# Kernel optimization log

Measured on AMD Instinct MI355X. Metric: run time of the kernel, lower is better.

Reference implementation:

```python
import jax, jax.numpy as jnp
import numpy as np

B, T, C, D, P = 8, 512, 32, 128, 1024
EPS = 1e-5

def setup_inputs() -> dict:
    key = jax.random.key(0)
    ks = jax.random.split(key, 11)
    s = 1.0 / np.sqrt(D)
    inp = {
        'x': jax.random.normal(ks[0], (B, T, C, D), jnp.float32),
        'x_mask': jax.random.randint(ks[1], (B, T, C), 0, 2) == 1,
        'p_mask': jax.random.randint(ks[2], (B, T, C), 0, 2) == 1,
        'pos': jax.random.randint(ks[3], (B, T, C), 0, P),
        'pe': jax.random.normal(ks[4], (P, D // 2, 2), jnp.float32),  # complex rpe as [re, im]
        'imp': jax.random.randint(ks[5], (B, T), 0, C),
        'idx_c': jax.random.randint(ks[6], (B, T, C), 0, C),
        'wq_w': jax.random.normal(ks[7], (D, D), jnp.float32) * s,
        'wq_b': jnp.zeros((D,), jnp.float32),
        'wk_w': jax.random.normal(ks[8], (D, D), jnp.float32) * s,
        'wk_b': jnp.zeros((D,), jnp.float32),
        'wv_w': jax.random.normal(ks[9], (D, D), jnp.float32) * s,
        'wv_b': jnp.zeros((D,), jnp.float32),
        'ls_gamma': 1e-5 * jnp.ones((D,), jnp.float32),
        'ln_gamma': jnp.ones((D,), jnp.float32),
        'ln_beta': jnp.zeros((D,), jnp.float32),
    }
    return inp


def _rotate(z, r):
    # z: (b,t,c,d) real; r: (b,t,c,d/2,2) complex multiplier [re,im]
    b, t, c, d = z.shape
    zr = z.reshape(b, t, c, d // 2, 2)
    re = zr[..., 0] * r[..., 0] - zr[..., 1] * r[..., 1]
    im = zr[..., 0] * r[..., 1] + zr[..., 1] * r[..., 0]
    return jnp.stack([re, im], axis=-1).reshape(b, t, c, d)


def reference(x, x_mask, p_mask, pos, pe, imp, idx_c,
              wq_w, wq_b, wk_w, wk_b, wv_w, wv_b,
              ls_gamma, ln_gamma, ln_beta):
    b, t, c, d = x.shape
    # channel selection gather: where x_mask, use per-token important channel
    imp_rep = jnp.broadcast_to(imp[:, :, None], (b, t, c))
    idx = jnp.where(x_mask, imp_rep, idx_c)            # (b,t,c)
    xg = jnp.take_along_axis(x, idx[..., None], axis=2)  # (b,t,c,d)
    # QKV projections (torch Linear: x @ W.T + b)
    q = xg @ wq_w.T + wq_b
    k = xg @ wk_w.T + wk_b
    v = xg @ wv_w.T + wv_b
    # relative PE complex rotation on q,k
    r = pe[pos]                                        # (b,t,c,d/2,2)
    q = _rotate(q, r)
    k = _rotate(k, r)
    # (b,c,t,d) layout; channel acts as head
    qt = q.transpose(0, 2, 1, 3)
    kt = k.transpose(0, 2, 1, 3)
    vt = v.transpose(0, 2, 1, 3)
    scores = jnp.einsum('bcqd,bckd->bcqk', qt, kt) / jnp.sqrt(jnp.float32(d))
    pm = p_mask.transpose(0, 2, 1)                     # (b,c,t)
    mask = pm[:, :, :, None] | pm[:, :, None, :]       # (b,c,t,t)
    attn = jax.nn.softmax(jnp.where(mask, -jnp.inf, scores), axis=-1)
    attn = jnp.nan_to_num(attn)
    xm = x_mask.transpose(0, 2, 1)                     # (b,c,t)
    weight = jnp.where(xm, 1.0 / t, 1.0)
    out = jnp.einsum('bcmn,bcnd->bmcd', attn * weight[:, :, None, :], vt)  # (b,t,c,d)
    # norm_first=False: LN(x + layer_scale(out))
    y = x + ls_gamma * out
    mu = jnp.mean(y, axis=-1, keepdims=True)
    var = jnp.mean(jnp.square(y - mu), axis=-1, keepdims=True)
    return (y - mu) / jnp.sqrt(var + EPS) * ln_gamma + ln_beta
```

## Files before the change

kernel.cpp:

```cpp
#include <hip/hip_runtime.h>
#include <hip/hip_bf16.h>

#define Bb 8
#define Tt 512
#define Cc 32
#define Dd 128
#define SCALE 0.08838834764831845f
#define SROW 520

typedef unsigned int u32;
typedef __hip_bfloat16 bf16;
typedef __attribute__((ext_vector_type(8))) short short8;
typedef __attribute__((ext_vector_type(4))) short short4v;
typedef __attribute__((ext_vector_type(4))) float floatx4;

__device__ __forceinline__ short f2bf(float f) {
    __hip_bfloat16 h = __float2bfloat16(f);
    return *(short*)&h;
}
__device__ __forceinline__ float bf2f(short s) {
    return __uint_as_float(((u32)(unsigned short)s) << 16);
}

__global__ __launch_bounds__(256)
void k_wconv(const float* __restrict__ wq, const float* __restrict__ wk,
             const float* __restrict__ wv, short* __restrict__ Wb)
{
    int g = blockIdx.x * 256 + threadIdx.x;
    int mat = g >> 14, rem = g & 16383;
    const float* src = (mat == 0) ? wq : (mat == 1) ? wk : wv;
    Wb[g] = f2bf(src[rem]);
}

__global__ __launch_bounds__(256)
void k_qkvm(const float* __restrict__ x, const int* __restrict__ xm,
            const int* __restrict__ pos, const float* __restrict__ pe,
            const int* __restrict__ imp, const int* __restrict__ idxc,
            const short* __restrict__ Wb,
            const float* __restrict__ bq, const float* __restrict__ bk,
            const float* __restrict__ bv,
            short* __restrict__ qb, short* __restrict__ kb, short* __restrict__ vb)
{
    const int R0  = blockIdx.x * 64;
    const int b   = R0 >> 14;
    const int t0  = (R0 >> 5) & 511;
    const int tid = threadIdx.x;
    const int w    = tid >> 6;
    const int lane = tid & 63;
    const int quad = lane >> 4;
    const int m    = lane & 15;

    __shared__ short xg[64 * 136];
    __shared__ short ot[64 * 392];

#pragma unroll
    for (int i = 0; i < 8; ++i) {
        int u   = tid + i * 256;
        int row = u >> 5, seg = u & 31;
        int R   = R0 + row;
        int idx = xm[R] ? imp[R >> 5] : idxc[R];
        float4 v = *(const float4*)(x + ((long)(R >> 5) * Cc + idx) * Dd + seg * 4);
        short4v s = {f2bf(v.x), f2bf(v.y), f2bf(v.z), f2bf(v.w)};
        *(short4v*)&xg[row * 136 + seg * 4] = s;
    }

    short8 wf[6][4];
    float  bias_v[6];
#pragma unroll
    for (int mat = 0; mat < 3; ++mat) {
        const float* bp = (mat == 0) ? bq : (mat == 1) ? bk : bv;
#pragma unroll
        for (int h = 0; h < 2; ++h) {
            int sl = mat * 2 + h;
            int ct = h * 4 + w;
            bias_v[sl] = bp[ct * 16 + m];
#pragma unroll
            for (int kk = 0; kk < 4; ++kk)
                wf[sl][kk] = *(const short8*)(Wb + ((long)mat * 128 + ct * 16 + m) * 128
                                              + kk * 32 + quad * 8);
        }
    }
    __syncthreads();

    for (int rt = 0; rt < 4; ++rt) {
        short8 af[4];
#pragma unroll
        for (int kk = 0; kk < 4; ++kk)
            af[kk] = *(const short8*)&xg[(rt * 16 + m) * 136 + kk * 32 + quad * 8];

        floatx4 acc[6];
#pragma unroll
        for (int sl = 0; sl < 6; ++sl) acc[sl] = (floatx4){0.f, 0.f, 0.f, 0.f};
#pragma unroll
        for (int kk = 0; kk < 4; ++kk)
#pragma unroll
            for (int sl = 0; sl < 6; ++sl)
                acc[sl] = __builtin_amdgcn_mfma_f32_16x16x32_bf16(af[kk], wf[sl][kk], acc[sl], 0, 0, 0);

        int po[4];
#pragma unroll
        for (int r = 0; r < 4; ++r) po[r] = pos[R0 + rt * 16 + quad * 4 + r];

#pragma unroll
        for (int sl = 0; sl < 6; ++sl) {
            int mat = sl >> 1;
            int ct  = (sl & 1) * 4 + w;
            int d   = ct * 16 + m;
#pragma unroll
            for (int r = 0; r < 4; ++r) {
                float v = acc[sl][r] + bias_v[sl];
                float p = __shfl_xor(v, 1, 64);
                if (mat < 2) {
                    const float* rp = pe + ((long)po[r] * (Dd / 2) + (d >> 1)) * 2;
                    float r0 = rp[0], r1 = rp[1];
                    v = (d & 1) ? fmaf(p, r1, v * r0) : fmaf(v, r0, -(p * r1));
                    if (mat == 0) v *= SCALE;
                }
                ot[(rt * 16 + quad * 4 + r) * 392 + mat * 128 + d] = f2bf(v);
            }
        }
    }
    __syncthreads();

    short* const mats[3] = {qb, kb, vb};
#pragma unroll
    for (int mat = 0; mat < 3; ++mat) {
        short* dst = mats[mat];
#pragma unroll
        for (int i = 0; i < 4; ++i) {
            int g = tid + i * 256;
            int n = g >> 4, off = (g & 15) * 8;
            int c = n & 31, tl = n >> 5;
            *(short8*)(dst + (((long)(b * Cc + c) * Tt) + t0 + tl) * Dd + off) =
                *(const short8*)&ot[n * 392 + mat * 128 + off];
        }
    }
}

__global__ __launch_bounds__(256)
void k_vt(const short* __restrict__ vb, const int* __restrict__ xm,
          short* __restrict__ vt)
{
    const int head = blockIdx.y;
    const int b    = head >> 5;
    const int c    = head & 31;
    const int t0   = blockIdx.x * 64;
    const int tid  = threadIdx.x;

    __shared__ short tile[64 * 136];
    __shared__ float wks[64];

    if (tid < 64)
        wks[tid] = xm[((long)b * Tt + t0 + tid) * Cc + c] ? (1.0f / Tt) : 1.0f;

    const short* src = vb + ((long)head * Tt + t0) * Dd;
#pragma unroll
    for (int i = 0; i < 4; ++i) {
        int u = tid + i * 256;
        int row = u >> 4, col8 = u & 15;
        int c8 = col8 ^ ((row >> 3) & 7);
        *(short8*)&tile[row * 136 + c8 * 8] = *(const short8*)(src + row * Dd + col8 * 8);
    }
    __syncthreads();

    short* dst = vt + (long)head * Dd * Tt + t0;
#pragma unroll
    for (int i = 0; i < 4; ++i) {
        int u = tid + i * 256;
        int d = u >> 3, t8 = (u & 7) * 8;
        int key = u & 7;
        int cs = ((d >> 3) ^ key) * 8 + (d & 7);
        short8 v;
#pragma unroll
        for (int j = 0; j < 8; ++j)
            v[j] = f2bf(bf2f(tile[(t8 + j) * 136 + cs]) * wks[t8 + j]);
        *(short8*)(dst + (long)d * Tt + t8) = v;
    }
}

__global__ __launch_bounds__(512, 4)
void k_attn(const short* __restrict__ qb, const short* __restrict__ kbp,
            const short* __restrict__ vtp, const float* __restrict__ x,
            const int* __restrict__ pm,
            const float* __restrict__ lsg, const float* __restrict__ lng,
            const float* __restrict__ lnb, float* __restrict__ out)
{
    const int l    = blockIdx.y * 256 + blockIdx.x;
    const int xcd  = l & 7;
    const int sws  = l >> 3;
    const int hh   = sws & 7;
    const int tl   = (sws >> 3) & 7;
    const int gg   = sws >> 6;
    const int head = xcd + ((gg * 8 + hh) << 3);
    const int b    = head >> 5;
    const int c    = head & 31;
    const int qt0  = tl * 64;
    const int tid  = threadIdx.x;
    const int w    = tid >> 6;
    const int lane = tid & 63;
    const int quad = lane >> 4;
    const int m    = lane & 15;

    __shared__ short S[64 * SROW];
    __shared__ u32   pkbits[16];
    __shared__ float rlS[64];
    __shared__ float ps1[8][64];
    __shared__ float ps2[8][64];
    __shared__ float mrs[64][2];

    {
        bool v = pm[((long)b * Tt + tid) * Cc + c] != 0;
        unsigned long long bal = __ballot(v);
        if (lane == 0) {
            pkbits[w * 2]     = (u32)bal;
            pkbits[w * 2 + 1] = (u32)(bal >> 32);
        }
    }

    short8 qf[4][4];
#pragma unroll
    for (int qt = 0; qt < 4; ++qt)
#pragma unroll
        for (int kk = 0; kk < 4; ++kk)
            qf[qt][kk] = *(const short8*)(qb + ((long)head * Tt + qt0 + qt * 16 + m) * Dd
                                          + kk * 32 + quad * 8);
    __syncthreads();

    for (int ch = 0; ch < 4; ++ch) {
        int kt = ch * 128 + w * 16 + m;
        const short* kp = kbp + ((long)head * Tt + kt) * Dd + quad * 8;
        floatx4 sc[4];
#pragma unroll
        for (int qt = 0; qt < 4; ++qt) sc[qt] = (floatx4){0.f, 0.f, 0.f, 0.f};
#pragma unroll
        for (int kk = 0; kk < 4; ++kk) {
            short8 bk = *(const short8*)(kp + kk * 32);
#pragma unroll
            for (int qt = 0; qt < 4; ++qt)
                sc[qt] = __builtin_amdgcn_mfma_f32_16x16x32_bf16(qf[qt][kk], bk, sc[qt], 0, 0, 0);
        }
        bool masked = (pkbits[kt >> 5] >> (kt & 31)) & 1;
#pragma unroll
        for (int qt = 0; qt < 4; ++qt)
#pragma unroll
            for (int r = 0; r < 4; ++r)
                S[(qt * 16 + quad * 4 + r) * SROW + kt] = f2bf(masked ? -1e30f : sc[qt][r]);
    }
    __syncthreads();

    {
        int qi = tid >> 3, part = tid & 7;
        short* rowp = &S[qi * SROW + part * 8];
        short8 sv[8];
#pragma unroll
        for (int j = 0; j < 8; ++j) sv[j] = *(short8*)&rowp[j * 64];
        float mx = -1e30f;
#pragma unroll
        for (int j = 0; j < 8; ++j)
#pragma unroll
            for (int e = 0; e < 8; ++e) mx = fmaxf(mx, bf2f(sv[j][e]));
        mx = fmaxf(mx, __shfl_xor(mx, 1, 64));
        mx = fmaxf(mx, __shfl_xor(mx, 2, 64));
        mx = fmaxf(mx, __shfl_xor(mx, 4, 64));
        float lsum = 0.f;
#pragma unroll
        for (int j = 0; j < 8; ++j)
#pragma unroll
            for (int e = 0; e < 8; ++e) {
                float s = bf2f(sv[j][e]);
                float ex = (s <= -1e29f) ? 0.f : __expf(s - mx);
                sv[j][e] = f2bf(ex);
                lsum += ex;
            }
#pragma unroll
        for (int j = 0; j < 8; ++j) *(short8*)&rowp[j * 64] = sv[j];
        lsum += __shfl_xor(lsum, 1, 64);
        lsum += __shfl_xor(lsum, 2, 64);
        lsum += __shfl_xor(lsum, 4, 64);
        if (part == 0) {
            int t = qt0 + qi;
            bool qmask = (pkbits[t >> 5] >> (t & 31)) & 1;
            rlS[qi] = (lsum > 0.f && !qmask) ? 1.0f / lsum : 0.f;
        }
    }
    __syncthreads();

    floatx4 oa[4];
#pragma unroll
    for (int qt = 0; qt < 4; ++qt) oa[qt] = (floatx4){0.f, 0.f, 0.f, 0.f};

    const short* vbase = vtp + (long)head * Dd * Tt + ((long)(w * 16 + m)) * Tt + quad * 8;
    for (int kv = 0; kv < 16; ++kv) {
        short8 bv = *(const short8*)(vbase + kv * 32);
#pragma unroll
        for (int qt = 0; qt < 4; ++qt) {
            short8 ap = *(const short8*)&S[(qt * 16 + m) * SROW + kv * 32 + quad * 8];
            oa[qt] = __builtin_amdgcn_mfma_f32_16x16x32_bf16(ap, bv, oa[qt], 0, 0, 0);
        }
    }

    const int d = w * 16 + m;
    const float lg = lsg[d];
    float yv[4][4];
    float s1[4][4], s2[4][4];
#pragma unroll
    for (int qt = 0; qt < 4; ++qt)
#pragma unroll
        for (int r = 0; r < 4; ++r) {
            int row = qt * 16 + quad * 4 + r;
            int t = qt0 + row;
            float val = oa[qt][r] * rlS[row];
            float y = x[(((long)b * Tt + t) * Cc + c) * Dd + d] + lg * val;
            yv[qt][r] = y;
            s1[qt][r] = y;
            s2[qt][r] = y * y;
        }
#pragma unroll
    for (int qt = 0; qt < 4; ++qt)
#pragma unroll
        for (int r = 0; r < 4; ++r) {
            float a = s1[qt][r], bb = s2[qt][r];
            a += __shfl_xor(a, 1, 64); bb += __shfl_xor(bb, 1, 64);
            a += __shfl_xor(a, 2, 64); bb += __shfl_xor(bb, 2, 64);
            a += __shfl_xor(a, 4, 64); bb += __shfl_xor(bb, 4, 64);
            a += __shfl_xor(a, 8, 64); bb += __shfl_xor(bb, 8, 64);
            if (m == 0) {
                ps1[w][qt * 16 + quad * 4 + r] = a;
                ps2[w][qt * 16 + quad * 4 + r] = bb;
            }
        }
    __syncthreads();
    if (tid < 64) {
        float a = 0.f, bb = 0.f;
#pragma unroll
        for (int wv = 0; wv < 8; ++wv) { a += ps1[wv][tid]; bb += ps2[wv][tid]; }
        float mean = a * (1.0f / Dd);
        float var  = bb * (1.0f / Dd) - mean * mean;
        mrs[tid][0] = mean;
        mrs[tid][1] = rsqrtf(var + 1e-5f);
    }
    __syncthreads();

    const float g = lng[d], be = lnb[d];
#pragma unroll
    for (int qt = 0; qt < 4; ++qt)
#pragma unroll
        for (int r = 0; r < 4; ++r) {
            int row = qt * 16 + quad * 4 + r;
            int t = qt0 + row;
            out[(((long)b * Tt + t) * Cc + c) * Dd + d] =
                (yv[qt][r] - mrs[row][0]) * mrs[row][1] * g + be;
        }
}

extern "C" void kernel_launch(void* const* d_in, const int* in_sizes, int n_in,
                              void* d_out, int out_size, void* d_ws, size_t ws_size,
                              hipStream_t stream) {
    const float* x    = (const float*)d_in[0];
    const int* xmask  = (const int*)d_in[1];
    const int* pmask  = (const int*)d_in[2];
    const int* pos    = (const int*)d_in[3];
    const float* pe   = (const float*)d_in[4];
    const int* imp    = (const int*)d_in[5];
    const int* idxc   = (const int*)d_in[6];
    const float* wq_w = (const float*)d_in[7];
    const float* wq_b = (const float*)d_in[8];
    const float* wk_w = (const float*)d_in[9];
    const float* wk_b = (const float*)d_in[10];
    const float* wv_w = (const float*)d_in[11];
    const float* wv_b = (const float*)d_in[12];
    const float* lsg  = (const float*)d_in[13];
    const float* lng  = (const float*)d_in[14];
    const float* lnb  = (const float*)d_in[15];
    float* out = (float*)d_out;

    size_t n = (size_t)Bb * Cc * Tt * Dd;
    short* qb = (short*)d_ws;
    short* kb = qb + n;
    short* vb = kb + n;
    short* vt = vb + n;
    short* Wb = vt + n;

    k_wconv<<<dim3(3 * Dd * Dd / 256), dim3(256), 0, stream>>>(wq_w, wk_w, wv_w, Wb);
    k_qkvm<<<dim3(Bb * Tt * Cc / 64), dim3(256), 0, stream>>>(
        x, xmask, pos, pe, imp, idxc, Wb, wq_b, wk_b, wv_b, qb, kb, vb);
    k_vt<<<dim3(Tt / 64, Bb * Cc), dim3(256), 0, stream>>>(vb, xmask, vt);
    k_attn<<<dim3(256, 8), dim3(512), 0, stream>>>(
        qb, kb, vt, x, pmask, lsg, lng, lnb, out);
}
```

Before: 313.5 us.

## Split attention over two key halves with online softmax to halve LDS score buffer

Processes keys in two halves of 256, keeping a running max and sum per query row and rescaling the output accumulator between halves, so the shared score tile shrinks by half. The aim is to let more blocks reside per CU by reducing LDS usage, and the launch bounds are raised accordingly. It adds extra barriers and rescale work, and the tighter launch bounds may pressure registers.

After: 588.9 us. +87.8%, slower.

```diff
diff --git a/kernel.cpp b/kernel.cpp
--- a/kernel.cpp
+++ b/kernel.cpp
@@ -6,7 +6,7 @@
 #define Cc 32
 #define Dd 128
 #define SCALE 0.08838834764831845f
-#define SROW 520
+#define SROW2 264
 
 typedef unsigned int u32;
 typedef __hip_bfloat16 bf16;
@@ -178,7 +178,7 @@
     }
 }
 
-__global__ __launch_bounds__(512, 4)
+__global__ __launch_bounds__(512, 8)
 void k_attn(const short* __restrict__ qb, const short* __restrict__ kbp,
             const short* __restrict__ vtp, const float* __restrict__ x,
             const int* __restrict__ pm,
@@ -201,9 +201,10 @@
     const int quad = lane >> 4;
     const int m    = lane & 15;
 
-    __shared__ short S[64 * SROW];
+    __shared__ short S[64 * SROW2];
     __shared__ u32   pkbits[16];
     __shared__ float rlS[64];
+    __shared__ float alS[64];
     __shared__ float ps1[8][64];
     __shared__ float ps2[8][64];
     __shared__ float mrs[64][2];
@@ -226,83 +227,101 @@
                                           + kk * 32 + quad * 8);
     __syncthreads();
 
-    for (int ch = 0; ch < 4; ++ch) {
-        int kt = ch * 128 + w * 16 + m;
-        const short* kp = kbp + ((long)head * Tt + kt) * Dd + quad * 8;
-        floatx4 sc[4];
-#pragma unroll
-        for (int qt = 0; qt < 4; ++qt) sc[qt] = (floatx4){0.f, 0.f, 0.f, 0.f};
-#pragma unroll
-        for (int kk = 0; kk < 4; ++kk) {
-            short8 bk = *(const short8*)(kp + kk * 32);
+    const short* vbase = vtp + (long)head * Dd * Tt + ((long)(w * 16 + m)) * Tt + quad * 8;
+
+    floatx4 oa[4];
+#pragma unroll
+    for (int qt = 0; qt < 4; ++qt) oa[qt] = (floatx4){0.f, 0.f, 0.f, 0.f};
+
+    float m_run = -1e30f, l_run = 0.f;
+
+    for (int hk = 0; hk < 2; ++hk) {
+        for (int ch = 0; ch < 2; ++ch) {
+            int ktl = ch * 128 + w * 16 + m;
+            int kt  = hk * 256 + ktl;
+            const short* kp = kbp + ((long)head * Tt + kt) * Dd + quad * 8;
+            floatx4 sc[4];
+#pragma unroll
+            for (int qt = 0; qt < 4; ++qt) sc[qt] = (floatx4){0.f, 0.f, 0.f, 0.f};
+#pragma unroll
+            for (int kk = 0; kk < 4; ++kk) {
+                short8 bk = *(const short8*)(kp + kk * 32);
+#pragma unroll
+                for (int qt = 0; qt < 4; ++qt)
+                    sc[qt] = __builtin_amdgcn_mfma_f32_16x16x32_bf16(qf[qt][kk], bk, sc[qt], 0, 0, 0);
+            }
+            bool masked = (pkbits[kt >> 5] >> (kt & 31)) & 1;
 #pragma unroll
             for (int qt = 0; qt < 4; ++qt)
-                sc[qt] = __builtin_amdgcn_mfma_f32_16x16x32_bf16(qf[qt][kk], bk, sc[qt], 0, 0, 0);
-        }
-        bool masked = (pkbits[kt >> 5] >> (kt & 31)) & 1;
+#pragma unroll
+                for (int r = 0; r < 4; ++r)
+                    S[(qt * 16 + quad * 4 + r) * SROW2 + ktl] = f2bf(masked ? -1e30f : sc[qt][r]);
+        }
+        __syncthreads();
+
+        {
+            int qi = tid >> 3, part = tid & 7;
+            short* rowp = &S[qi * SROW2 + part * 8];
+            short8 sv[4];
+#pragma unroll
+            for (int j = 0; j < 4; ++j) sv[j] = *(short8*)&rowp[j * 64];
+            float mx = -1e30f;
+#pragma unroll
+            for (int j = 0; j < 4; ++j)
+#pragma unroll
+                for (int e = 0; e < 8; ++e) mx = fmaxf(mx, bf2f(sv[j][e]));
+            mx = fmaxf(mx, __shfl_xor(mx, 1, 64));
+            mx = fmaxf(mx, __shfl_xor(mx, 2, 64));
+            mx = fmaxf(mx, __shfl_xor(mx, 4, 64));
+            float m_new = fmaxf(m_run, mx);
+            float lsum = 0.f;
+#pragma unroll
+            for (int j = 0; j < 4; ++j)
+#pragma unroll
+                for (int e = 0; e < 8; ++e) {
+                    float s = bf2f(sv[j][e]);
+                    float ex = (s <= -1e29f) ? 0.f : __expf(s - m_new);
+                    sv[j][e] = f2bf(ex);
+                    lsum += ex;
+                }
+#pragma unroll
+            for (int j = 0; j < 4; ++j) *(short8*)&rowp[j * 64] = sv[j];
+            lsum += __shfl_xor(lsum, 1, 64);
+            lsum += __shfl_xor(lsum, 2, 64);
+            lsum += __shfl_xor(lsum, 4, 64);
+            float al = __expf(m_run - m_new);
+            l_run = l_run * al + lsum;
+            m_run = m_new;
+            if (part == 0) {
+                alS[qi] = al;
+                if (hk == 1) {
+                    int t = qt0 + qi;
+                    bool qmask = (pkbits[t >> 5] >> (t & 31)) & 1;
+                    rlS[qi] = (l_run > 0.f && !qmask) ? 1.0f / l_run : 0.f;
+                }
+            }
+        }
+        __syncthreads();
+
 #pragma unroll
         for (int qt = 0; qt < 4; ++qt)
 #pragma unroll
             for (int r = 0; r < 4; ++r)
-                S[(qt * 16 + quad * 4 + r) * SROW + kt] = f2bf(masked ? -1e30f : sc[qt][r]);
-    }
-    __syncthreads();
-
-    {
-        int qi = tid >> 3, part = tid & 7;
-        short* rowp = &S[qi * SROW + part * 8];
-        short8 sv[8];
-#pragma unroll
-        for (int j = 0; j < 8; ++j) sv[j] = *(short8*)&rowp[j * 64];
-        float mx = -1e30f;
-#pragma unroll
-        for (int j = 0; j < 8; ++j)
-#pragma unroll
-            for (int e = 0; e < 8; ++e) mx = fmaxf(mx, bf2f(sv[j][e]));
-        mx = fmaxf(mx, __shfl_xor(mx, 1, 64));
-        mx = fmaxf(mx, __shfl_xor(mx, 2, 64));
-        mx = fmaxf(mx, __shfl_xor(mx, 4, 64));
-        float lsum = 0.f;
-#pragma unroll
-        for (int j = 0; j < 8; ++j)
-#pragma unroll
-            for (int e = 0; e < 8; ++e) {
-                float s = bf2f(sv[j][e]);
-                float ex = (s <= -1e29f) ? 0.f : __expf(s - mx);
-                sv[j][e] = f2bf(ex);
-                lsum += ex;
+                oa[qt][r] *= alS[qt * 16 + quad * 4 + r];
+        for (int kv = 0; kv < 8; ++kv) {
+            short8 bv = *(const short8*)(vbase + (hk * 8 + kv) * 32);
+#pragma unroll
+            for (int qt = 0; qt < 4; ++qt) {
+                short8 ap = *(const short8*)&S[(qt * 16 + m) * SROW2 + kv * 32 + quad * 8];
+                oa[qt] = __builtin_amdgcn_mfma_f32_16x16x32_bf16(ap, bv, oa[qt], 0, 0, 0);
             }
-#pragma unroll
-        for (int j = 0; j < 8; ++j) *(short8*)&rowp[j * 64] = sv[j];
-        lsum += __shfl_xor(lsum, 1, 64);
-        lsum += __shfl_xor(lsum, 2, 64);
-        lsum += __shfl_xor(lsum, 4, 64);
-        if (part == 0) {
-            int t = qt0 + qi;
-            bool qmask = (pkbits[t >> 5] >> (t & 31)) & 1;
-            rlS[qi] = (lsum > 0.f && !qmask) ? 1.0f / lsum : 0.f;
-        }
-    }
-    __syncthreads();
-
-    floatx4 oa[4];
-#pragma unroll
-    for (int qt = 0; qt < 4; ++qt) oa[qt] = (floatx4){0.f, 0.f, 0.f, 0.f};
-
-    const short* vbase = vtp + (long)head * Dd * Tt + ((long)(w * 16 + m)) * Tt + quad * 8;
-    for (int kv = 0; kv < 16; ++kv) {
-        short8 bv = *(const short8*)(vbase + kv * 32);
-#pragma unroll
-        for (int qt = 0; qt < 4; ++qt) {
-            short8 ap = *(const short8*)&S[(qt * 16 + m) * SROW + kv * 32 + quad * 8];
-            oa[qt] = __builtin_amdgcn_mfma_f32_16x16x32_bf16(ap, bv, oa[qt], 0, 0, 0);
-        }
+        }
+        __syncthreads();
     }
 
     const int d = w * 16 + m;
     const float lg = lsg[d];
     float yv[4][4];
-    float s1[4][4], s2[4][4];
 #pragma unroll
     for (int qt = 0; qt < 4; ++qt)
 #pragma unroll
@@ -312,14 +331,12 @@
             float val = oa[qt][r] * rlS[row];
             float y = x[(((long)b * Tt + t) * Cc + c) * Dd + d] + lg * val;
             yv[qt][r] = y;
-            s1[qt][r] = y;
-            s2[qt][r] = y * y;
         }
 #pragma unroll
     for (int qt = 0; qt < 4; ++qt)
 #pragma unroll
         for (int r = 0; r < 4; ++r) {
-            float a = s1[qt][r], bb = s2[qt][r];
+            float a = yv[qt][r], bb = yv[qt][r] * yv[qt][r];
             a += __shfl_xor(a, 1, 64); bb += __shfl_xor(bb, 1, 64);
             a += __shfl_xor(a, 2, 64); bb += __shfl_xor(bb, 2, 64);
             a += __shfl_xor(a, 4, 64); bb += __shfl_xor(bb, 4, 64);
```

## Fuse V projection into transpose kernel, dropping intermediate V buffer

Applied to the files above, without the earlier changes.

Removes V computation from the QKV kernel and computes V in the transpose kernel directly from a fresh gather of x, applying the x_mask weight before writing the transposed bf16 V. This eliminates writing and re-reading a full intermediate V buffer. In exchange, x is gathered a second time in fp32 and the V GEMM runs in a separate kernel with less weight reuse.

Result: slower. 355.0 us (+13.2%).

```diff
diff --git a/kernel.cpp b/kernel.cpp
--- a/kernel.cpp
+++ b/kernel.cpp
@@ -7,6 +7,7 @@
 #define Dd 128
 #define SCALE 0.08838834764831845f
 #define SROW 520
+#define OROW 264
 
 typedef unsigned int u32;
 typedef __hip_bfloat16 bf16;
@@ -38,8 +39,7 @@
             const int* __restrict__ imp, const int* __restrict__ idxc,
             const short* __restrict__ Wb,
             const float* __restrict__ bq, const float* __restrict__ bk,
-            const float* __restrict__ bv,
-            short* __restrict__ qb, short* __restrict__ kb, short* __restrict__ vb)
+            short* __restrict__ qb, short* __restrict__ kb)
 {
     const int R0  = blockIdx.x * 64;
     const int b   = R0 >> 14;
@@ -51,7 +51,7 @@
     const int m    = lane & 15;
 
     __shared__ short xg[64 * 136];
-    __shared__ short ot[64 * 392];
+    __shared__ short ot[64 * OROW];
 
 #pragma unroll
     for (int i = 0; i < 8; ++i) {
@@ -64,11 +64,11 @@
         *(short4v*)&xg[row * 136 + seg * 4] = s;
     }
 
-    short8 wf[6][4];
-    float  bias_v[6];
-#pragma unroll
-    for (int mat = 0; mat < 3; ++mat) {
-        const float* bp = (mat == 0) ? bq : (mat == 1) ? bk : bv;
+    short8 wf[4][4];
+    float  bias_v[4];
+#pragma unroll
+    for (int mat = 0; mat < 2; ++mat) {
+        const float* bp = (mat == 0) ? bq : bk;
 #pragma unroll
         for (int h = 0; h < 2; ++h) {
             int sl = mat * 2 + h;
@@ -88,13 +88,13 @@
         for (int kk = 0; kk < 4; ++kk)
             af[kk] = *(const short8*)&xg[(rt * 16 + m) * 136 + kk * 32 + quad * 8];
 
-        floatx4 acc[6];
-#pragma unroll
-        for (int sl = 0; sl < 6; ++sl) acc[sl] = (floatx4){0.f, 0.f, 0.f, 0.f};
-#pragma unroll
-        for (int kk = 0; kk < 4; ++kk)
-#pragma unroll
-            for (int sl = 0; sl < 6; ++sl)
+        floatx4 acc[4];
+#pragma unroll
+        for (int sl = 0; sl < 4; ++sl) acc[sl] = (floatx4){0.f, 0.f, 0.f, 0.f};
+#pragma unroll
+        for (int kk = 0; kk < 4; ++kk)
+#pragma unroll
+            for (int sl = 0; sl < 4; ++sl)
                 acc[sl] = __builtin_amdgcn_mfma_f32_16x16x32_bf16(af[kk], wf[sl][kk], acc[sl], 0, 0, 0);
 
         int po[4];
@@ -102,7 +102,7 @@
         for (int r = 0; r < 4; ++r) po[r] = pos[R0 + rt * 16 + quad * 4 + r];
 
 #pragma unroll
-        for (int sl = 0; sl < 6; ++sl) {
+        for (int sl = 0; sl < 4; ++sl) {
             int mat = sl >> 1;
             int ct  = (sl & 1) * 4 + w;
             int d   = ct * 16 + m;
@@ -110,21 +110,19 @@
             for (int r = 0; r < 4; ++r) {
                 float v = acc[sl][r] + bias_v[sl];
                 float p = __shfl_xor(v, 1, 64);
-                if (mat < 2) {
-                    const float* rp = pe + ((long)po[r] * (Dd / 2) + (d >> 1)) * 2;
-                    float r0 = rp[0], r1 = rp[1];
-                    v = (d & 1) ? fmaf(p, r1, v * r0) : fmaf(v, r0, -(p * r1));
-                    if (mat == 0) v *= SCALE;
-                }
-                ot[(rt * 16 + quad * 4 + r) * 392 + mat * 128 + d] = f2bf(v);
+                const float* rp = pe + ((long)po[r] * (Dd / 2) + (d >> 1)) * 2;
+                float r0 = rp[0], r1 = rp[1];
+                v = (d & 1) ? fmaf(p, r1, v * r0) : fmaf(v, r0, -(p * r1));
+                if (mat == 0) v *= SCALE;
+                ot[(rt * 16 + quad * 4 + r) * OROW + mat * 128 + d] = f2bf(v);
             }
         }
     }
     __syncthreads();
 
-    short* const mats[3] = {qb, kb, vb};
-#pragma unroll
-    for (int mat = 0; mat < 3; ++mat) {
+    short* const mats[2] = {qb, kb};
+#pragma unroll
+    for (int mat = 0; mat < 2; ++mat) {
         short* dst = mats[mat];
 #pragma unroll
         for (int i = 0; i < 4; ++i) {
@@ -132,34 +130,86 @@
             int n = g >> 4, off = (g & 15) * 8;
             int c = n & 31, tl = n >> 5;
             *(short8*)(dst + (((long)(b * Cc + c) * Tt) + t0 + tl) * Dd + off) =
-                *(const short8*)&ot[n * 392 + mat * 128 + off];
+                *(const short8*)&ot[n * OROW + mat * 128 + off];
         }
     }
 }
 
 __global__ __launch_bounds__(256)
-void k_vt(const short* __restrict__ vb, const int* __restrict__ xm,
-          short* __restrict__ vt)
+void k_v(const float* __restrict__ x, const int* __restrict__ xm,
+         const int* __restrict__ imp, const int* __restrict__ idxc,
+         const short* __restrict__ Wb, const float* __restrict__ bvp,
+         short* __restrict__ vt)
 {
     const int head = blockIdx.y;
     const int b    = head >> 5;
     const int c    = head & 31;
     const int t0   = blockIdx.x * 64;
     const int tid  = threadIdx.x;
-
+    const int w    = tid >> 6;
+    const int lane = tid & 63;
+    const int quad = lane >> 4;
+    const int m    = lane & 15;
+
+    __shared__ short xg[64 * 136];
     __shared__ short tile[64 * 136];
     __shared__ float wks[64];
 
-    if (tid < 64)
-        wks[tid] = xm[((long)b * Tt + t0 + tid) * Cc + c] ? (1.0f / Tt) : 1.0f;
-
-    const short* src = vb + ((long)head * Tt + t0) * Dd;
-#pragma unroll
-    for (int i = 0; i < 4; ++i) {
-        int u = tid + i * 256;
-        int row = u >> 4, col8 = u & 15;
-        int c8 = col8 ^ ((row >> 3) & 7);
-        *(short8*)&tile[row * 136 + c8 * 8] = *(const short8*)(src + row * Dd + col8 * 8);
+#pragma unroll
+    for (int i = 0; i < 8; ++i) {
+        int u   = tid + i * 256;
+        int row = u >> 5, seg = u & 31;
+        long tr = (long)b * Tt + t0 + row;
+        long R  = tr * Cc + c;
+        int xmv = xm[R];
+        int idx = xmv ? imp[tr] : idxc[R];
+        float4 v = *(const float4*)(x + (tr * Cc + idx) * Dd + seg * 4);
+        short4v s = {f2bf(v.x), f2bf(v.y), f2bf(v.z), f2bf(v.w)};
+        *(short4v*)&xg[row * 136 + seg * 4] = s;
+        if (seg == 0) wks[row] = xmv ? (1.0f / Tt) : 1.0f;
+    }
+
+    short8 wf[2][4];
+    float  bias_v[2];
+#pragma unroll
+    for (int h = 0; h < 2; ++h) {
+        int ct = h * 4 + w;
+        bias_v[h] = bvp[ct * 16 + m];
+#pragma unroll
+        for (int kk = 0; kk < 4; ++kk)
+            wf[h][kk] = *(const short8*)(Wb + ((long)2 * 128 + ct * 16 + m) * 128
+                                         + kk * 32 + quad * 8);
+    }
+    __syncthreads();
+
+#pragma unroll
+    for (int rt = 0; rt < 4; ++rt) {
+        short8 af[4];
+#pragma unroll
+        for (int kk = 0; kk < 4; ++kk)
+            af[kk] = *(const short8*)&xg[(rt * 16 + m) * 136 + kk * 32 + quad * 8];
+
+        floatx4 acc[2];
+        acc[0] = (floatx4){0.f, 0.f, 0.f, 0.f};
+        acc[1] = (floatx4){0.f, 0.f, 0.f, 0.f};
+#pragma unroll
+        for (int kk = 0; kk < 4; ++kk)
+#pragma unroll
+            for (int h = 0; h < 2; ++h)
+                acc[h] = __builtin_amdgcn_mfma_f32_16x16x32_bf16(af[kk], wf[h][kk], acc[h], 0, 0, 0);
+
+#pragma unroll
+        for (int h = 0; h < 2; ++h) {
+            int ct = h * 4 + w;
+            int d  = ct * 16 + m;
+#pragma unroll
+            for (int r = 0; r < 4; ++r) {
+                int row = rt * 16 + quad * 4 + r;
+                float v = (acc[h][r] + bias_v[h]) * wks[row];
+                int c8 = (d >> 3) ^ ((row >> 3) & 7);
+                tile[row * 136 + c8 * 8 + (d & 7)] = f2bf(v);
+            }
+        }
     }
     __syncthreads();
 
@@ -173,7 +223,7 @@
         short8 v;
 #pragma unroll
         for (int j = 0; j < 8; ++j)
-            v[j] = f2bf(bf2f(tile[(t8 + j) * 136 + cs]) * wks[t8 + j]);
+            v[j] = tile[(t8 + j) * 136 + cs];
         *(short8*)(dst + (long)d * Tt + t8) = v;
     }
 }
@@ -377,14 +427,14 @@
     size_t n = (size_t)Bb * Cc * Tt * Dd;
     short* qb = (short*)d_ws;
     short* kb = qb + n;
-    short* vb = kb + n;
-    short* vt = vb + n;
+    short* vt = kb + n;
     short* Wb = vt + n;
 
     k_wconv<<<dim3(3 * Dd * Dd / 256), dim3(256), 0, stream>>>(wq_w, wk_w, wv_w, Wb);
     k_qkvm<<<dim3(Bb * Tt * Cc / 64), dim3(256), 0, stream>>>(
-        x, xmask, pos, pe, imp, idxc, Wb, wq_b, wk_b, wv_b, qb, kb, vb);
-    k_vt<<<dim3(Tt / 64, Bb * Cc), dim3(256), 0, stream>>>(vb, xmask, vt);
+        x, xmask, pos, pe, imp, idxc, Wb, wq_b, wk_b, qb, kb);
+    k_v<<<dim3(Tt / 64, Bb * Cc), dim3(256), 0, stream>>>(
+        x, xmask, imp, idxc, Wb, wv_b, vt);
     k_attn<<<dim3(256, 8), dim3(512), 0, stream>>>(
         qb, kb, vt, x, pmask, lsg, lng, lnb, out);
 }
```
